# Performance work log

Measured on AMD Instinct MI355X. Metric: run time of the kernel, lower is better.

## Reference

```python
import jax, jax.numpy as jnp
import numpy as np

N = 50000      # nodes
E = 800000     # edges
D_IN = 512     # input feature dim
H1, C1 = 8, 8  # conv1: heads, per-head channels -> 64 concat
D_MID = H1 * C1
D_OUT = 64     # output_dim (classes)


def _lin(key, din, dout):
    # torch.nn.Linear default init: U(-1/sqrt(din), 1/sqrt(din))
    kw, kb = jax.random.split(key)
    s = 1.0 / np.sqrt(din)
    W = jax.random.uniform(kw, (din, dout), minval=-s, maxval=s, dtype=jnp.float32)
    b = jax.random.uniform(kb, (dout,), minval=-s, maxval=s, dtype=jnp.float32)
    return W, b


def setup_inputs() -> dict:
    key = jax.random.key(0)
    ks = jax.random.split(key, 10)
    x = jax.random.normal(ks[0], (N, D_IN), dtype=jnp.float32)
    edge_index = jax.random.randint(ks[1], (2, E), 0, N, dtype=jnp.int64)
    Wq1, bq1 = _lin(ks[2], D_IN, D_MID)
    Wk1, bk1 = _lin(ks[3], D_IN, D_MID)
    Wv1, bv1 = _lin(ks[4], D_IN, D_MID)
    Ws1, bs1 = _lin(ks[5], D_IN, D_MID)          # skip (concat=True -> heads*out)
    Wq2, bq2 = _lin(ks[6], D_MID, D_OUT)
    Wk2, bk2 = _lin(ks[7], D_MID, D_OUT)
    Wv2, bv2 = _lin(ks[8], D_MID, D_OUT)
    Ws2, bs2 = _lin(ks[9], D_MID, D_OUT)         # skip (concat=False -> out)
    return dict(x=x, edge_index=edge_index,
                Wq1=Wq1, bq1=bq1, Wk1=Wk1, bk1=bk1, Wv1=Wv1, bv1=bv1, Ws1=Ws1, bs1=bs1,
                Wq2=Wq2, bq2=bq2, Wk2=Wk2, bk2=bk2, Wv2=Wv2, bv2=bv2, Ws2=Ws2, bs2=bs2)


def transformer_conv(x, src, dst, Wq, bq, Wk, bk, Wv, bv, Ws, bs, heads, out_ch, concat):
    # PyG TransformerConv (edge_dim=None, beta=False, root_weight=True), eval mode
    n = x.shape[0]
    q = (x @ Wq + bq).reshape(n, heads, out_ch)
    k = (x @ Wk + bk).reshape(n, heads, out_ch)
    v = (x @ Wv + bv).reshape(n, heads, out_ch)
    # per-edge scaled dot-product attention logits [E, H]
    alpha = jnp.einsum('ehc,ehc->eh', q[dst], k[src]) / np.sqrt(out_ch)
    # scatter-softmax over incoming edges of each target node
    amax = jax.ops.segment_max(alpha, dst, num_segments=n)            # [N, H]
    ex = jnp.exp(alpha - amax[dst])
    denom = jax.ops.segment_sum(ex, dst, num_segments=n)              # [N, H]
    a = ex / (denom[dst] + 1e-16)                                     # [E, H]
    # weighted scatter-add of values
    out = jax.ops.segment_sum(a[:, :, None] * v[src], dst, num_segments=n)  # [N, H, C]
    out = out.reshape(n, heads * out_ch) if concat else out.mean(axis=1)
    return out + (x @ Ws + bs)  # root/skip connection


def reference(x, edge_index, Wq1, bq1, Wk1, bk1, Wv1, bv1, Ws1, bs1,
              Wq2, bq2, Wk2, bk2, Wv2, bv2, Ws2, bs2):
    src, dst = edge_index[0], edge_index[1]   # message flows j=src -> i=dst
    # dropout layers are no-ops in eval mode
    h = transformer_conv(x, src, dst, Wq1, bq1, Wk1, bk1, Wv1, bv1, Ws1, bs1, H1, C1, True)
    h = jax.nn.elu(h)
    h = transformer_conv(h, src, dst, Wq2, bq2, Wk2, bk2, Wv2, bv2, Ws2, bs2, 1, D_OUT, False)
    return jax.nn.log_softmax(h, axis=-1)
```

## Files before the change

kernel.cpp:

```cpp
#include <hip/hip_runtime.h>
#include <hip/hip_bf16.h>
#include <math.h>


typedef __attribute__((ext_vector_type(4))) float f32x4;
typedef __attribute__((ext_vector_type(8))) short bf16x8;
typedef __attribute__((ext_vector_type(8))) unsigned short u16x8;

__device__ inline unsigned short f2bf(float f) {
    union { float f; unsigned u; } v; v.f = f;
    unsigned r = (v.u + 0x7fffu + ((v.u >> 16) & 1u)) >> 16;
    return (unsigned short)r;
}
__device__ inline float bf2f(unsigned short u) {
    union { unsigned u; float f; } v; v.u = ((unsigned)u) << 16; return v.f;
}

#define NEGBIG (-1e30f)

__global__ void prep_w(const float* __restrict__ W0, const float* __restrict__ b0,
                       const float* __restrict__ W1, const float* __restrict__ b1,
                       const float* __restrict__ W2, const float* __restrict__ b2,
                       const float* __restrict__ W3, const float* __restrict__ b3,
                       int K, unsigned short* __restrict__ Bt, float* __restrict__ bias) {
    int i = blockIdx.x * 256 + threadIdx.x;
    int tot = 4 * K * 64;
    if (i < tot) {
        int which = i / (K * 64);
        int rem = i - which * K * 64;
        int k = rem >> 6, n = rem & 63;
        const float* W = (which == 0) ? W0 : (which == 1) ? W1 : (which == 2) ? W2 : W3;
        Bt[(size_t)(which * 64 + n) * K + k] = f2bf(W[k * 64 + n]);
    }
    if (i < 256) {
        int which = i >> 6;
        const float* b = (which == 0) ? b0 : (which == 1) ? b1 : (which == 2) ? b2 : b3;
        bias[i] = b[i & 63];
    }
}

template<int KSTEPS, bool ABF16>
__global__ __launch_bounds__(256) void gemm_mfma(const void* __restrict__ Av, int M,
                                                 const unsigned short* __restrict__ Bt,
                                                 const float* __restrict__ bias,
                                                 float* __restrict__ out) {
    constexpr int K = KSTEPS * 64;
    __shared__ unsigned short As[2][64][72];
    const int tid = threadIdx.x;
    const int lane = tid & 63;
    const int w = tid >> 6;
    const int node0 = blockIdx.x * 64;
    const int r16 = lane & 15, g = lane >> 4;

    f32x4 acc[4][4] = {};

    const int srow = tid >> 2;
    const int sc0 = (tid & 3) * 16;
    const int node = node0 + srow;
    const bool nvalid = node < M;

    float4 f0, f1, f2, f3;
    u16x8 a0, a1;

#define ISSUE_LOAD(KS)                                                                     \
    do {                                                                                   \
        if (ABF16) {                                                                       \
            a0 = (u16x8){}; a1 = (u16x8){};                                                \
            if (nvalid) {                                                                  \
                const u16x8* p = (const u16x8*)((const unsigned short*)Av +                \
                                  (size_t)node * K + (KS) * 64 + sc0);                     \
                a0 = p[0]; a1 = p[1];                                                      \
            }                                                                              \
        } else {                                                                           \
            f0 = make_float4(0.f, 0.f, 0.f, 0.f); f1 = f0; f2 = f0; f3 = f0;               \
            if (nvalid) {                                                                  \
                const float4* p = (const float4*)((const float*)Av +                       \
                                   (size_t)node * K + (KS) * 64 + sc0);                    \
                f0 = p[0]; f1 = p[1]; f2 = p[2]; f3 = p[3];                                \
            }                                                                              \
        }                                                                                  \
    } while (0)

#define WRITE_LDS(BUF)                                                                     \
    do {                                                                                   \
        unsigned short t[16];                                                              \
        if (ABF16) {                                                                       \
            _Pragma("unroll")                                                              \
            for (int j = 0; j < 8; ++j) { t[j] = a0[j]; t[8 + j] = a1[j]; }                \
        } else {                                                                           \
            t[0] = f2bf(f0.x); t[1] = f2bf(f0.y); t[2] = f2bf(f0.z); t[3] = f2bf(f0.w);    \
            t[4] = f2bf(f1.x); t[5] = f2bf(f1.y); t[6] = f2bf(f1.z); t[7] = f2bf(f1.w);    \
            t[8] = f2bf(f2.x); t[9] = f2bf(f2.y); t[10] = f2bf(f2.z); t[11] = f2bf(f2.w);  \
            t[12] = f2bf(f3.x); t[13] = f2bf(f3.y); t[14] = f2bf(f3.z); t[15] = f2bf(f3.w);\
        }                                                                                  \
        u16x8 w0, w1;                                                                      \
        _Pragma("unroll")                                                                  \
        for (int j = 0; j < 8; ++j) { w0[j] = t[j]; w1[j] = t[8 + j]; }                    \
        *(u16x8*)&As[BUF][srow][sc0] = w0;                                                 \
        *(u16x8*)&As[BUF][srow][sc0 + 8] = w1;                                             \
    } while (0)

    ISSUE_LOAD(0);
    WRITE_LDS(0);
    __syncthreads();

#pragma unroll
    for (int ks = 0; ks < KSTEPS; ++ks) {
        bf16x8 bfr[8];
#pragma unroll
        for (int kk = 0; kk < 2; ++kk)
#pragma unroll
            for (int ni = 0; ni < 4; ++ni)
                bfr[kk * 4 + ni] = *(const bf16x8*)&Bt[(size_t)(w * 64 + ni * 16 + r16) * K
                                                        + ks * 64 + kk * 32 + g * 8];
        if (ks + 1 < KSTEPS) ISSUE_LOAD(ks + 1);

#pragma unroll
        for (int kk = 0; kk < 2; ++kk) {
            bf16x8 afr[4];
#pragma unroll
            for (int mi = 0; mi < 4; ++mi)
                afr[mi] = *(const bf16x8*)&As[ks & 1][mi * 16 + r16][kk * 32 + g * 8];
#pragma unroll
            for (int ni = 0; ni < 4; ++ni)
#pragma unroll
                for (int mi = 0; mi < 4; ++mi)
                    acc[mi][ni] = __builtin_amdgcn_mfma_f32_16x16x32_bf16(
                        afr[mi], bfr[kk * 4 + ni], acc[mi][ni], 0, 0, 0);
        }

        if (ks + 1 < KSTEPS) WRITE_LDS((ks + 1) & 1);
        __syncthreads();
    }
#undef ISSUE_LOAD
#undef WRITE_LDS

#pragma unroll
    for (int mi = 0; mi < 4; ++mi) {
#pragma unroll
        for (int r = 0; r < 4; ++r) {
            int row = node0 + mi * 16 + g * 4 + r;
            if (row < M) {
                size_t o = (size_t)row * 256 + w * 64;
#pragma unroll
                for (int ni = 0; ni < 4; ++ni)
                    out[o + ni * 16 + r16] = acc[mi][ni][r] + bias[w * 64 + ni * 16 + r16];
            }
        }
    }
}

__global__ void pack_kv(const float* __restrict__ qkvs, unsigned short* __restrict__ kvt,
                        int n32) {
    int i = blockIdx.x * 256 + threadIdx.x;
    if (i >= n32) return;
    int node = i >> 5, c4 = (i & 31) * 4;
    float4 f = *(const float4*)&qkvs[(size_t)node * 256 + 64 + c4];
    ushort4 o;
    o.x = f2bf(f.x); o.y = f2bf(f.y); o.z = f2bf(f.z); o.w = f2bf(f.w);
    *(ushort4*)&kvt[(size_t)node * 128 + c4] = o;
}

__global__ void zero2(int* __restrict__ a, int* __restrict__ b, int n) {
    int i = blockIdx.x * 256 + threadIdx.x;
    if (i < n) { a[i] = 0; b[i] = 0; }
}

__global__ void hist_deg(const int* __restrict__ dst, int E, int N, int* __restrict__ deg) {
    int e = blockIdx.x * 256 + threadIdx.x;
    if (e >= E) return;
    int d = dst[e];
    if ((unsigned)d < (unsigned)N) atomicAdd(&deg[d], 1);
}

__global__ __launch_bounds__(256) void scan_blk_k(const int* __restrict__ deg, int N,
                                                  int* __restrict__ rowptr,
                                                  int* __restrict__ blk_sums) {
    __shared__ int wsum[4];
    const int t = threadIdx.x;
    const int base = blockIdx.x * 1024 + t * 4;
    int d0 = 0, d1 = 0, d2 = 0, d3 = 0;
    if (base + 3 < N) {
        int4 v = *(const int4*)&deg[base];
        d0 = v.x; d1 = v.y; d2 = v.z; d3 = v.w;
    } else {
        if (base < N)     d0 = deg[base];
        if (base + 1 < N) d1 = deg[base + 1];
        if (base + 2 < N) d2 = deg[base + 2];
    }
    int s = d0 + d1 + d2 + d3;
    int incl = s;
    const int lane = t & 63, w = t >> 6;
#pragma unroll
    for (int off = 1; off < 64; off <<= 1) {
        int v = __shfl_up(incl, off, 64);
        if (lane >= off) incl += v;
    }
    if (lane == 63) wsum[w] = incl;
    __syncthreads();
    int woff = 0;
    if (w > 0) woff += wsum[0];
    if (w > 1) woff += wsum[1];
    if (w > 2) woff += wsum[2];
    int excl = woff + incl - s;
    if (base < N)     rowptr[base]     = excl;
    if (base + 1 < N) rowptr[base + 1] = excl + d0;
    if (base + 2 < N) rowptr[base + 2] = excl + d0 + d1;
    if (base + 3 < N) rowptr[base + 3] = excl + d0 + d1 + d2;
    if (t == 255) blk_sums[blockIdx.x] = woff + incl;
}

__global__ __launch_bounds__(64) void scan_top_k(const int* __restrict__ blk_sums,
                                                 int* __restrict__ blk_off, int nblk,
                                                 int* __restrict__ rowptrN) {
    const int lane = threadIdx.x;
    int carry = 0;
    for (int b = 0; b < nblk; b += 64) {
        int idx = b + lane;
        int v = (idx < nblk) ? blk_sums[idx] : 0;
        int incl = v;
#pragma unroll
        for (int off = 1; off < 64; off <<= 1) {
            int u = __shfl_up(incl, off, 64);
            if (lane >= off) incl += u;
        }
        if (idx < nblk) blk_off[idx] = carry + incl - v;
        carry += __shfl(incl, 63, 64);
    }
    if (lane == 0) *rowptrN = carry;
}

__global__ __launch_bounds__(256) void scan_add_k(int* __restrict__ rowptr,
                                                  const int* __restrict__ blk_off, int N) {
    const int base = blockIdx.x * 1024 + threadIdx.x * 4;
    const int off = blk_off[blockIdx.x];
    if (base + 3 < N) {
        int4 v = *(int4*)&rowptr[base];
        v.x += off; v.y += off; v.z += off; v.w += off;
        *(int4*)&rowptr[base] = v;
    } else {
        for (int i = 0; i < 4; ++i)
            if (base + i < N) rowptr[base + i] += off;
    }
}

__global__ void scatter_edges(const int* __restrict__ src, const int* __restrict__ dst,
                              int E, int N,
                              const int* __restrict__ rowptr, int* __restrict__ cursor,
                              int* __restrict__ csr_src) {
    int e = blockIdx.x * 256 + threadIdx.x;
    if (e >= E) return;
    int d = dst[e];
    if ((unsigned)d >= (unsigned)N) return;
    int slot = rowptr[d] + atomicAdd(&cursor[d], 1);
    if ((unsigned)slot < (unsigned)E) csr_src[slot] = src[e];
}

__global__ __launch_bounds__(256) void attn1(const float* __restrict__ qkvs,
                                             const unsigned short* __restrict__ kvt,
                                             const int* __restrict__ rowptr,
                                             const int* __restrict__ csr_src,
                                             unsigned short* __restrict__ h1bf, int N) {
    int node = blockIdx.x * 4 + (threadIdx.x >> 6);
    if (node >= N) return;
    const int lane = threadIdx.x & 63;
    const int g = lane >> 3, h = lane & 7;

    float q[8];
    {
        const float4* qp = (const float4*)(qkvs + (size_t)node * 256 + h * 8);
        float4 qa = qp[0], qb = qp[1];
        q[0] = qa.x; q[1] = qa.y; q[2] = qa.z; q[3] = qa.w;
        q[4] = qb.x; q[5] = qb.y; q[6] = qb.z; q[7] = qb.w;
    }

    const float SC = 1.44269504f * 0.35355339059327373f;
    float m = NEGBIG, l = 0.f;
    float a[8] = {};

    const int beg = rowptr[node], end = rowptr[node + 1];
    const int nt = (end - beg + 7) >> 3;

    for (int t = 0; t < nt; ++t) {
        int idx = beg + t * 8 + g;
        bool act = idx < end;
        int s = csr_src[act ? idx : beg];
        s = ((unsigned)s < (unsigned)N) ? s : 0;
        const unsigned short* kb = kvt + (size_t)s * 128 + h * 8;
        u16x8 ku = *(const u16x8*)kb;
        u16x8 vu = *(const u16x8*)(kb + 64);
        float p = q[0] * bf2f(ku[0]) + q[1] * bf2f(ku[1])
                + q[2] * bf2f(ku[2]) + q[3] * bf2f(ku[3])
                + q[4] * bf2f(ku[4]) + q[5] * bf2f(ku[5])
                + q[6] * bf2f(ku[6]) + q[7] * bf2f(ku[7]);
        float x = act ? (p * SC) : NEGBIG;
        float mnew = fmaxf(m, x);
        float corr = exp2f(m - mnew);
        float wgt = act ? exp2f(x - mnew) : 0.f;
        l = l * corr + wgt;
#pragma unroll
        for (int i = 0; i < 8; ++i) a[i] = a[i] * corr + wgt * bf2f(vu[i]);
        m = mnew;
    }

#pragma unroll
    for (int off = 8; off <= 32; off <<= 1) {
        float mo = __shfl_xor(m, off, 64);
        float lo = __shfl_xor(l, off, 64);
        float mn = fmaxf(m, mo);
        float s1 = exp2f(m - mn);
        float s2 = exp2f(mo - mn);
        l = l * s1 + lo * s2;
#pragma unroll
        for (int i = 0; i < 8; ++i) {
            float ao = __shfl_xor(a[i], off, 64);
            a[i] = a[i] * s1 + ao * s2;
        }
        m = mn;
    }

    if (g == 0) {
        float inv = 1.f / (l + 1e-16f);
        const float4* sp = (const float4*)(qkvs + (size_t)node * 256 + 192 + h * 8);
        float4 s0 = sp[0], s1v = sp[1];
        float svv[8] = { s0.x, s0.y, s0.z, s0.w, s1v.x, s1v.y, s1v.z, s1v.w };
        u16x8 o;
#pragma unroll
        for (int i = 0; i < 8; ++i) {
            float t = a[i] * inv + svv[i];
            t = (t > 0.f) ? t : expm1f(t);
            o[i] = f2bf(t);
        }
        *(u16x8*)(h1bf + (size_t)node * 64 + h * 8) = o;
    }
}

__global__ __launch_bounds__(256) void attn2(const float* __restrict__ qkvs,
                                             const unsigned short* __restrict__ kvt,
                                             const int* __restrict__ rowptr,
                                             const int* __restrict__ csr_src,
                                             float* __restrict__ out, int N) {
    int node = blockIdx.x * 4 + (threadIdx.x >> 6);
    if (node >= N) return;
    const int lane = threadIdx.x & 63;
    const int g = lane >> 4, j = lane & 15;

    float4 qv = *(const float4*)&qkvs[(size_t)node * 256 + j * 4];
    const float SC = 1.44269504f * 0.125f;
    float m = NEGBIG, l = 0.f;
    float4 acc = make_float4(0.f, 0.f, 0.f, 0.f);

    const int beg = rowptr[node], end = rowptr[node + 1];
    const int nt = (end - beg + 3) >> 2;

    for (int t = 0; t < nt; ++t) {
        int idx = beg + t * 4 + g;
        bool act = idx < end;
        int s = csr_src[act ? idx : beg];
        s = ((unsigned)s < (unsigned)N) ? s : 0;
        const unsigned short* kb = kvt + (size_t)s * 128 + j * 4;
        ushort4 ku = *(const ushort4*)kb;
        ushort4 vu = *(const ushort4*)(kb + 64);
        float p = qv.x * bf2f(ku.x) + qv.y * bf2f(ku.y)
                + qv.z * bf2f(ku.z) + qv.w * bf2f(ku.w);
        p += __shfl_xor(p, 1, 64);
        p += __shfl_xor(p, 2, 64);
        p += __shfl_xor(p, 4, 64);
        p += __shfl_xor(p, 8, 64);
        float x = act ? (p * SC) : NEGBIG;
        float mnew = fmaxf(m, x);
        float corr = exp2f(m - mnew);
        float wgt = act ? exp2f(x - mnew) : 0.f;
        l = l * corr + wgt;
        acc.x = acc.x * corr + wgt * bf2f(vu.x);
        acc.y = acc.y * corr + wgt * bf2f(vu.y);
        acc.z = acc.z * corr + wgt * bf2f(vu.z);
        acc.w = acc.w * corr + wgt * bf2f(vu.w);
        m = mnew;
    }

#pragma unroll
    for (int off = 16; off <= 32; off <<= 1) {
        float mo = __shfl_xor(m, off, 64);
        float lo = __shfl_xor(l, off, 64);
        float ax = __shfl_xor(acc.x, off, 64);
        float ay = __shfl_xor(acc.y, off, 64);
        float az = __shfl_xor(acc.z, off, 64);
        float aw = __shfl_xor(acc.w, off, 64);
        float mn = fmaxf(m, mo);
        float s1 = exp2f(m - mn);
        float s2 = exp2f(mo - mn);
        l = l * s1 + lo * s2;
        acc.x = acc.x * s1 + ax * s2;
        acc.y = acc.y * s1 + ay * s2;
        acc.z = acc.z * s1 + az * s2;
        acc.w = acc.w * s1 + aw * s2;
        m = mn;
    }

    float4 sv = *(const float4*)&qkvs[(size_t)node * 256 + 192 + j * 4];
    float inv = 1.f / (l + 1e-16f);
    float4 t4;
    t4.x = acc.x * inv + sv.x;
    t4.y = acc.y * inv + sv.y;
    t4.z = acc.z * inv + sv.z;
    t4.w = acc.w * inv + sv.w;

    float mx = fmaxf(fmaxf(t4.x, t4.y), fmaxf(t4.z, t4.w));
#pragma unroll
    for (int off = 1; off <= 8; off <<= 1) mx = fmaxf(mx, __shfl_xor(mx, off, 64));
    float es = expf(t4.x - mx) + expf(t4.y - mx) + expf(t4.z - mx) + expf(t4.w - mx);
#pragma unroll
    for (int off = 1; off <= 8; off <<= 1) es += __shfl_xor(es, off, 64);
    float ls = logf(es);
    if (g == 0) {
        float4 o;
        o.x = (t4.x - mx) - ls;
        o.y = (t4.y - mx) - ls;
        o.z = (t4.z - mx) - ls;
        o.w = (t4.w - mx) - ls;
        *(float4*)&out[(size_t)node * 64 + j * 4] = o;
    }
}

extern "C" void kernel_launch(void* const* d_in, const int* in_sizes, int n_in,
                              void* d_out, int out_size, void* d_ws, size_t ws_size,
                              hipStream_t stream) {
    const int N = in_sizes[0] / 512;
    const int E = in_sizes[1] / 2;
    const float* x   = (const float*)d_in[0];
    const int*   ei  = (const int*)d_in[1];
    const int* src = ei;
    const int* dst = ei + E;
    const float *Wq1 = (const float*)d_in[2],  *bq1 = (const float*)d_in[3];
    const float *Wk1 = (const float*)d_in[4],  *bk1 = (const float*)d_in[5];
    const float *Wv1 = (const float*)d_in[6],  *bv1 = (const float*)d_in[7];
    const float *Ws1 = (const float*)d_in[8],  *bs1 = (const float*)d_in[9];
    const float *Wq2 = (const float*)d_in[10], *bq2 = (const float*)d_in[11];
    const float *Wk2 = (const float*)d_in[12], *bk2 = (const float*)d_in[13];
    const float *Wv2 = (const float*)d_in[14], *bv2 = (const float*)d_in[15];
    const float *Ws2 = (const float*)d_in[16], *bs2 = (const float*)d_in[17];

    auto align16 = [](size_t v) { return (v + 15) & ~(size_t)15; };

    const int nblk = (N + 1023) / 1024;

    float* ws = (float*)d_ws;
    const size_t OFF_QKVS = 0;
    const size_t OFF_H1B  = align16(OFF_QKVS + (size_t)N * 256);
    const size_t OFF_BT1  = align16(OFF_H1B  + (size_t)N * 32);
    const size_t OFF_BT2  = align16(OFF_BT1  + 65536);
    const size_t OFF_BI1  = align16(OFF_BT2  + 8192);
    const size_t OFF_BI2  = align16(OFF_BI1  + 256);
    const size_t OFF_ROWP = align16(OFF_BI2  + 256);
    const size_t OFF_DEG  = align16(OFF_ROWP + (size_t)N + 1);
    const size_t OFF_CUR  = align16(OFF_DEG  + (size_t)N);
    const size_t OFF_CSRC = align16(OFF_CUR  + (size_t)N);
    const size_t OFF_KVT  = align16(OFF_CSRC + (size_t)E);
    const size_t OFF_BSUM = align16(OFF_KVT  + (size_t)N * 64);
    const size_t OFF_BOFF = align16(OFF_BSUM + (size_t)nblk);
    const size_t TOTAL    = align16(OFF_BOFF + (size_t)nblk);
    if (ws_size < TOTAL * sizeof(float)) return;

    float* qkvs  = ws + OFF_QKVS;
    unsigned short* h1bf = (unsigned short*)(ws + OFF_H1B);
    unsigned short* bt1  = (unsigned short*)(ws + OFF_BT1);
    unsigned short* bt2  = (unsigned short*)(ws + OFF_BT2);
    float* bias1 = ws + OFF_BI1;
    float* bias2 = ws + OFF_BI2;
    int* rowptr  = (int*)(ws + OFF_ROWP);
    int* deg     = (int*)(ws + OFF_DEG);
    int* cursor  = (int*)(ws + OFF_CUR);
    int* csr_src = (int*)(ws + OFF_CSRC);
    unsigned short* kvt = (unsigned short*)(ws + OFF_KVT);
    int* blk_sums = (int*)(ws + OFF_BSUM);
    int* blk_off  = (int*)(ws + OFF_BOFF);
    float* out   = (float*)d_out;

    const int gBlocks = (N + 63) / 64;
    const int nBlocks4 = (N + 3) / 4;
    const int n32 = N * 32;

    prep_w<<<(4 * 512 * 64 + 255) / 256, 256, 0, stream>>>(
        Wq1, bq1, Wk1, bk1, Wv1, bv1, Ws1, bs1, 512, bt1, bias1);
    prep_w<<<(4 * 64 * 64 + 255) / 256, 256, 0, stream>>>(
        Wq2, bq2, Wk2, bk2, Wv2, bv2, Ws2, bs2, 64, bt2, bias2);

    zero2<<<(N + 255) / 256, 256, 0, stream>>>(deg, cursor, N);
    hist_deg<<<(E + 255) / 256, 256, 0, stream>>>(dst, E, N, deg);
    scan_blk_k<<<nblk, 256, 0, stream>>>(deg, N, rowptr, blk_sums);
    scan_top_k<<<1, 64, 0, stream>>>(blk_sums, blk_off, nblk, &rowptr[N]);
    scan_add_k<<<nblk, 256, 0, stream>>>(rowptr, blk_off, N);
    scatter_edges<<<(E + 255) / 256, 256, 0, stream>>>(src, dst, E, N, rowptr, cursor, csr_src);

    gemm_mfma<8, false><<<gBlocks, 256, 0, stream>>>(x, N, bt1, bias1, qkvs);
    pack_kv<<<(n32 + 255) / 256, 256, 0, stream>>>(qkvs, kvt, n32);
    attn1<<<nBlocks4, 256, 0, stream>>>(qkvs, kvt, rowptr, csr_src, h1bf, N);

    gemm_mfma<1, true><<<gBlocks, 256, 0, stream>>>(h1bf, N, bt2, bias2, qkvs);
    pack_kv<<<(n32 + 255) / 256, 256, 0, stream>>>(qkvs, kvt, n32);
    attn2<<<nBlocks4, 256, 0, stream>>>(qkvs, kvt, rowptr, csr_src, out, N);
}
```

Baseline: 267.5 us.

## Halve GEMM row tile to 32 and prefetch A two k-steps ahead

```diff
diff --git a/kernel.cpp b/kernel.cpp
--- a/kernel.cpp
+++ b/kernel.cpp
@@ -45,63 +45,58 @@
                                                  const float* __restrict__ bias,
                                                  float* __restrict__ out) {
     constexpr int K = KSTEPS * 64;
-    __shared__ unsigned short As[2][64][72];
+    __shared__ unsigned short As[2][32][72];
     const int tid = threadIdx.x;
     const int lane = tid & 63;
     const int w = tid >> 6;
-    const int node0 = blockIdx.x * 64;
+    const int node0 = blockIdx.x * 32;
     const int r16 = lane & 15, g = lane >> 4;
 
-    f32x4 acc[4][4] = {};
-
-    const int srow = tid >> 2;
-    const int sc0 = (tid & 3) * 16;
+    f32x4 acc[2][4] = {};
+
+    const int srow = tid >> 3;
+    const int col0 = (tid & 7) * 8;
     const int node = node0 + srow;
     const bool nvalid = node < M;
 
-    float4 f0, f1, f2, f3;
-    u16x8 a0, a1;
-
-#define ISSUE_LOAD(KS)                                                                     \
+    float4 fA[2][2];
+    u16x8 aA[2];
+
+#define ISSUE_LOAD(KS, SET)                                                                \
     do {                                                                                   \
         if (ABF16) {                                                                       \
-            a0 = (u16x8){}; a1 = (u16x8){};                                                \
-            if (nvalid) {                                                                  \
-                const u16x8* p = (const u16x8*)((const unsigned short*)Av +                \
-                                  (size_t)node * K + (KS) * 64 + sc0);                     \
-                a0 = p[0]; a1 = p[1];                                                      \
-            }                                                                              \
+            aA[SET] = (u16x8){};                                                           \
+            if (nvalid)                                                                    \
+                aA[SET] = *(const u16x8*)((const unsigned short*)Av +                      \
+                              (size_t)node * K + (KS) * 64 + col0);                        \
         } else {                                                                           \
-            f0 = make_float4(0.f, 0.f, 0.f, 0.f); f1 = f0; f2 = f0; f3 = f0;               \
+            fA[SET][0] = make_float4(0.f, 0.f, 0.f, 0.f);                                  \
+            fA[SET][1] = fA[SET][0];                                                       \
             if (nvalid) {                                                                  \
                 const float4* p = (const float4*)((const float*)Av +                       \
-                                   (size_t)node * K + (KS) * 64 + sc0);                    \
-                f0 = p[0]; f1 = p[1]; f2 = p[2]; f3 = p[3];                                \
+                                   (size_t)node * K + (KS) * 64 + col0);                   \
+                fA[SET][0] = p[0]; fA[SET][1] = p[1];                                      \
             }                                                                              \
         }                                                                                  \
     } while (0)
 
-#define WRITE_LDS(BUF)                                                                     \
+#define WRITE_LDS(BUF, SET)                                                                \
     do {                                                                                   \
-        unsigned short t[16];                                                              \
+        u16x8 t;                                                                           \
         if (ABF16) {                                                                       \
-            _Pragma("unroll")                                                              \
-            for (int j = 0; j < 8; ++j) { t[j] = a0[j]; t[8 + j] = a1[j]; }                \
+            t = aA[SET];                                                                   \
         } else {                                                                           \
-            t[0] = f2bf(f0.x); t[1] = f2bf(f0.y); t[2] = f2bf(f0.z); t[3] = f2bf(f0.w);    \
-            t[4] = f2bf(f1.x); t[5] = f2bf(f1.y); t[6] = f2bf(f1.z); t[7] = f2bf(f1.w);    \
-            t[8] = f2bf(f2.x); t[9] = f2bf(f2.y); t[10] = f2bf(f2.z); t[11] = f2bf(f2.w);  \
-            t[12] = f2bf(f3.x); t[13] = f2bf(f3.y); t[14] = f2bf(f3.z); t[15] = f2bf(f3.w);\
+            t[0] = f2bf(fA[SET][0].x); t[1] = f2bf(fA[SET][0].y);                          \
+            t[2] = f2bf(fA[SET][0].z); t[3] = f2bf(fA[SET][0].w);                          \
+            t[4] = f2bf(fA[SET][1].x); t[5] = f2bf(fA[SET][1].y);                          \
+            t[6] = f2bf(fA[SET][1].z); t[7] = f2bf(fA[SET][1].w);                          \
         }                                                                                  \
-        u16x8 w0, w1;                                                                      \
-        _Pragma("unroll")                                                                  \
-        for (int j = 0; j < 8; ++j) { w0[j] = t[j]; w1[j] = t[8 + j]; }                    \
-        *(u16x8*)&As[BUF][srow][sc0] = w0;                                                 \
-        *(u16x8*)&As[BUF][srow][sc0 + 8] = w1;                                             \
+        *(u16x8*)&As[BUF][srow][col0] = t;                                                 \
     } while (0)
 
-    ISSUE_LOAD(0);
-    WRITE_LDS(0);
+    ISSUE_LOAD(0, 0);
+    if (KSTEPS > 1) ISSUE_LOAD(1, 1);
+    WRITE_LDS(0, 0);
     __syncthreads();
 
 #pragma unroll
@@ -113,30 +108,30 @@
             for (int ni = 0; ni < 4; ++ni)
                 bfr[kk * 4 + ni] = *(const bf16x8*)&Bt[(size_t)(w * 64 + ni * 16 + r16) * K
                                                         + ks * 64 + kk * 32 + g * 8];
-        if (ks + 1 < KSTEPS) ISSUE_LOAD(ks + 1);
+        if (ks + 2 < KSTEPS) ISSUE_LOAD(ks + 2, ks & 1);
 
 #pragma unroll
         for (int kk = 0; kk < 2; ++kk) {
-            bf16x8 afr[4];
-#pragma unroll
-            for (int mi = 0; mi < 4; ++mi)
+            bf16x8 afr[2];
+#pragma unroll
+            for (int mi = 0; mi < 2; ++mi)
                 afr[mi] = *(const bf16x8*)&As[ks & 1][mi * 16 + r16][kk * 32 + g * 8];
 #pragma unroll
             for (int ni = 0; ni < 4; ++ni)
 #pragma unroll
-                for (int mi = 0; mi < 4; ++mi)
+                for (int mi = 0; mi < 2; ++mi)
                     acc[mi][ni] = __builtin_amdgcn_mfma_f32_16x16x32_bf16(
                         afr[mi], bfr[kk * 4 + ni], acc[mi][ni], 0, 0, 0);
         }
 
-        if (ks + 1 < KSTEPS) WRITE_LDS((ks + 1) & 1);
+        if (ks + 1 < KSTEPS) WRITE_LDS((ks + 1) & 1, (ks + 1) & 1);
         __syncthreads();
     }
 #undef ISSUE_LOAD
 #undef WRITE_LDS
 
 #pragma unroll
-    for (int mi = 0; mi < 4; ++mi) {
+    for (int mi = 0; mi < 2; ++mi) {
 #pragma unroll
         for (int r = 0; r < 4; ++r) {
             int row = node0 + mi * 16 + g * 4 + r;
@@ -477,7 +472,7 @@
     int* blk_off  = (int*)(ws + OFF_BOFF);
     float* out   = (float*)d_out;
 
-    const int gBlocks = (N + 63) / 64;
+    const int gBlocks = (N + 31) / 32;
     const int nBlocks4 = (N + 3) / 4;
     const int n32 = N * 32;
 
```

After: 281.5 us. 1.05x slower.

## Load GEMM A fragments directly from global memory, dropping LDS staging

Applied to the files above, without the earlier changes.

```diff
diff --git a/kernel.cpp b/kernel.cpp
--- a/kernel.cpp
+++ b/kernel.cpp
@@ -45,7 +45,6 @@
                                                  const float* __restrict__ bias,
                                                  float* __restrict__ out) {
     constexpr int K = KSTEPS * 64;
-    __shared__ unsigned short As[2][64][72];
     const int tid = threadIdx.x;
     const int lane = tid & 63;
     const int w = tid >> 6;
@@ -54,86 +53,56 @@
 
     f32x4 acc[4][4] = {};
 
-    const int srow = tid >> 2;
-    const int sc0 = (tid & 3) * 16;
-    const int node = node0 + srow;
-    const bool nvalid = node < M;
-
-    float4 f0, f1, f2, f3;
-    u16x8 a0, a1;
-
-#define ISSUE_LOAD(KS)                                                                     \
-    do {                                                                                   \
-        if (ABF16) {                                                                       \
-            a0 = (u16x8){}; a1 = (u16x8){};                                                \
-            if (nvalid) {                                                                  \
-                const u16x8* p = (const u16x8*)((const unsigned short*)Av +                \
-                                  (size_t)node * K + (KS) * 64 + sc0);                     \
-                a0 = p[0]; a1 = p[1];                                                      \
-            }                                                                              \
-        } else {                                                                           \
-            f0 = make_float4(0.f, 0.f, 0.f, 0.f); f1 = f0; f2 = f0; f3 = f0;               \
-            if (nvalid) {                                                                  \
-                const float4* p = (const float4*)((const float*)Av +                       \
-                                   (size_t)node * K + (KS) * 64 + sc0);                    \
-                f0 = p[0]; f1 = p[1]; f2 = p[2]; f3 = p[3];                                \
-            }                                                                              \
-        }                                                                                  \
-    } while (0)
-
-#define WRITE_LDS(BUF)                                                                     \
-    do {                                                                                   \
-        unsigned short t[16];                                                              \
-        if (ABF16) {                                                                       \
-            _Pragma("unroll")                                                              \
-            for (int j = 0; j < 8; ++j) { t[j] = a0[j]; t[8 + j] = a1[j]; }                \
-        } else {                                                                           \
-            t[0] = f2bf(f0.x); t[1] = f2bf(f0.y); t[2] = f2bf(f0.z); t[3] = f2bf(f0.w);    \
-            t[4] = f2bf(f1.x); t[5] = f2bf(f1.y); t[6] = f2bf(f1.z); t[7] = f2bf(f1.w);    \
-            t[8] = f2bf(f2.x); t[9] = f2bf(f2.y); t[10] = f2bf(f2.z); t[11] = f2bf(f2.w);  \
-            t[12] = f2bf(f3.x); t[13] = f2bf(f3.y); t[14] = f2bf(f3.z); t[15] = f2bf(f3.w);\
-        }                                                                                  \
-        u16x8 w0, w1;                                                                      \
-        _Pragma("unroll")                                                                  \
-        for (int j = 0; j < 8; ++j) { w0[j] = t[j]; w1[j] = t[8 + j]; }                    \
-        *(u16x8*)&As[BUF][srow][sc0] = w0;                                                 \
-        *(u16x8*)&As[BUF][srow][sc0 + 8] = w1;                                             \
-    } while (0)
-
-    ISSUE_LOAD(0);
-    WRITE_LDS(0);
-    __syncthreads();
-
-#pragma unroll
+    const unsigned short* Abf[4];
+    const float* Af[4];
+#pragma unroll
+    for (int mi = 0; mi < 4; ++mi) {
+        int row = node0 + mi * 16 + r16;
+        row = (row < M) ? row : (M - 1);
+        if (ABF16) Abf[mi] = (const unsigned short*)Av + (size_t)row * K;
+        else       Af[mi]  = (const float*)Av + (size_t)row * K;
+    }
+    const int colA = g * 8;
+
     for (int ks = 0; ks < KSTEPS; ++ks) {
-        bf16x8 bfr[8];
+        bf16x8 bfr[2][4];
 #pragma unroll
         for (int kk = 0; kk < 2; ++kk)
 #pragma unroll
             for (int ni = 0; ni < 4; ++ni)
-                bfr[kk * 4 + ni] = *(const bf16x8*)&Bt[(size_t)(w * 64 + ni * 16 + r16) * K
-                                                        + ks * 64 + kk * 32 + g * 8];
-        if (ks + 1 < KSTEPS) ISSUE_LOAD(ks + 1);
-
-#pragma unroll
-        for (int kk = 0; kk < 2; ++kk) {
-            bf16x8 afr[4];
-#pragma unroll
-            for (int mi = 0; mi < 4; ++mi)
-                afr[mi] = *(const bf16x8*)&As[ks & 1][mi * 16 + r16][kk * 32 + g * 8];
+                bfr[kk][ni] = *(const bf16x8*)&Bt[(size_t)(w * 64 + ni * 16 + r16) * K
+                                                   + ks * 64 + kk * 32 + g * 8];
+        bf16x8 afr[2][4];
+        if (ABF16) {
+#pragma unroll
+            for (int kk = 0; kk < 2; ++kk)
+#pragma unroll
+                for (int mi = 0; mi < 4; ++mi)
+                    afr[kk][mi] = *(const bf16x8*)&Abf[mi][ks * 64 + kk * 32 + colA];
+        } else {
+#pragma unroll
+            for (int kk = 0; kk < 2; ++kk)
+#pragma unroll
+                for (int mi = 0; mi < 4; ++mi) {
+                    const float4* p = (const float4*)&Af[mi][ks * 64 + kk * 32 + colA];
+                    float4 u = p[0], v = p[1];
+                    bf16x8 t;
+                    t[0] = (short)f2bf(u.x); t[1] = (short)f2bf(u.y);
+                    t[2] = (short)f2bf(u.z); t[3] = (short)f2bf(u.w);
+                    t[4] = (short)f2bf(v.x); t[5] = (short)f2bf(v.y);
+                    t[6] = (short)f2bf(v.z); t[7] = (short)f2bf(v.w);
+                    afr[kk][mi] = t;
+                }
+        }
+#pragma unroll
+        for (int kk = 0; kk < 2; ++kk)
 #pragma unroll
             for (int ni = 0; ni < 4; ++ni)
 #pragma unroll
                 for (int mi = 0; mi < 4; ++mi)
                     acc[mi][ni] = __builtin_amdgcn_mfma_f32_16x16x32_bf16(
-                        afr[mi], bfr[kk * 4 + ni], acc[mi][ni], 0, 0, 0);
-        }
-
-        if (ks + 1 < KSTEPS) WRITE_LDS((ks + 1) & 1);
-        __syncthreads();
-    }
-#undef ISSUE_LOAD
-#undef WRITE_LDS
+                        afr[kk][mi], bfr[kk][ni], acc[mi][ni], 0, 0, 0);
+    }
 
 #pragma unroll
     for (int mi = 0; mi < 4; ++mi) {
```

Result: slower. 320.4 us (+19.8%).
